# Performance work log

Measured on AMD Instinct MI355X. Metric: run time of the kernel, lower is better.

The kernel has to match this reference:

```python
import jax, jax.numpy as jnp
import numpy as np

EMBED = 1024
HEADS = 16
HEAD_DIM = EMBED // HEADS


def setup_inputs() -> dict:
    key = jax.random.key(0)
    ks = jax.random.split(key, 11)
    B, L, E = 2, 2048, EMBED
    s = 1.0 / np.sqrt(E)
    return {
        "query": jax.random.normal(ks[0], (B, L, E), jnp.float32),
        "key": jax.random.normal(ks[1], (B, L, E), jnp.float32),
        "value": jax.random.normal(ks[2], (B, L, E), jnp.float32),
        "Wq": jax.random.normal(ks[3], (E, E), jnp.float32) * s,
        "bq": jax.random.normal(ks[4], (E,), jnp.float32) * s,
        "Wk": jax.random.normal(ks[5], (E, E), jnp.float32) * s,
        "bk": jax.random.normal(ks[6], (E,), jnp.float32) * s,
        "Wv": jax.random.normal(ks[7], (E, E), jnp.float32) * s,
        "bv": jax.random.normal(ks[8], (E,), jnp.float32) * s,
        "Wo": jax.random.normal(ks[9], (E, E), jnp.float32) * s,
        "bo": jax.random.normal(ks[10], (E,), jnp.float32) * s,
    }


def reference(query, key, value, Wq, bq, Wk, bk, Wv, bv, Wo, bo):
    B, Lq, E = query.shape
    Lk = key.shape[1]
    # Linear projections (torch Linear: x @ W.T + b)
    q = (query @ Wq.T + bq).reshape(B, Lq, HEADS, HEAD_DIM).transpose(0, 2, 1, 3)
    k = (key @ Wk.T + bk).reshape(B, Lk, HEADS, HEAD_DIM).transpose(0, 2, 1, 3)
    v = (value @ Wv.T + bv).reshape(B, Lk, HEADS, HEAD_DIM).transpose(0, 2, 1, 3)
    # NOTE: original scales by sqrt(embed_size), not sqrt(head_dim)
    energy = jnp.einsum("bhqd,bhkd->bhqk", q, k) / jnp.sqrt(jnp.float32(E))
    attn = jax.nn.softmax(energy, axis=-1)
    out = jnp.einsum("bhqk,bhkd->bhqd", attn, v)  # [B,H,Lq,D]
    out = out.transpose(0, 2, 1, 3).reshape(B, Lq, E)
    return out @ Wo.T + bo
```

## Files before the change

### kernel.cpp

```cpp
#include <hip/hip_runtime.h>
#include <hip/hip_bf16.h>


typedef __attribute__((ext_vector_type(4))) float f32x4;
typedef __attribute__((ext_vector_type(16))) float f32x16;
typedef __attribute__((ext_vector_type(8))) short bf16x8;
typedef __attribute__((ext_vector_type(4))) short bf16x4;
typedef __attribute__((ext_vector_type(2))) unsigned int u32x2;

static __device__ __forceinline__ unsigned short f2bf(float f) {
  union { float f; unsigned int u; } a; a.f = f;
  unsigned int u = a.u;
  u += 0x7FFFu + ((u >> 16) & 1u);
  return (unsigned short)(u >> 16);
}

static __device__ __forceinline__ unsigned packrn(float lo, float hi) {
  __hip_bfloat162 h = __float22bfloat162_rn(float2{lo, hi});
  union { __hip_bfloat162 h; unsigned u; } c; c.h = h;
  return c.u;
}

static __device__ __forceinline__ unsigned pack2(float lo, float hi) {
  unsigned a = __float_as_uint(lo) + 0x8000u;
  unsigned b = __float_as_uint(hi) + 0x8000u;
  return __builtin_amdgcn_perm(b, a, 0x07060302);
}

static __device__ __forceinline__ unsigned xchg32(unsigned x) {
  u32x2 r = __builtin_amdgcn_permlane32_swap(x, x, false, false);
  return x ^ r[0] ^ r[1];
}

#define AS1(p) ((const __attribute__((address_space(1))) void*)(p))
#define AS3(p) ((__attribute__((address_space(3))) void*)(p))

__global__ __launch_bounds__(256) void cvt_kernel(
    const float* __restrict__ q, const float* __restrict__ k, const float* __restrict__ v,
    const float* __restrict__ wq, const float* __restrict__ wk, const float* __restrict__ wv,
    const float* __restrict__ wo, short* __restrict__ ws) {
  long i = (long)blockIdx.x * 256 + threadIdx.x;
  long e = i * 8;
  const float* src; long off;
  if (e < 12582912) {
    int s = (int)(e >> 22);
    src = s == 0 ? q : (s == 1 ? k : v);
    off = e & 4194303;
  } else {
    long e2 = e - 12582912;
    int s = (int)(e2 >> 20);
    src = s == 0 ? wq : (s == 1 ? wk : (s == 2 ? wv : wo));
    off = e2 & 1048575;
  }
  f32x4 a = *(const f32x4*)(src + off);
  f32x4 b = *(const f32x4*)(src + off + 4);
  bf16x8 o;
  o[0] = (short)f2bf(a[0]); o[1] = (short)f2bf(a[1]);
  o[2] = (short)f2bf(a[2]); o[3] = (short)f2bf(a[3]);
  o[4] = (short)f2bf(b[0]); o[5] = (short)f2bf(b[1]);
  o[6] = (short)f2bf(b[2]); o[7] = (short)f2bf(b[3]);
  *(bf16x8*)(ws + e) = o;
}

__device__ __forceinline__ void gemm_tile(const short* __restrict__ A, const short* __restrict__ B,
                                          int m0, int n0, f32x4 acc[4][4],
                                          short* As, short* Bs) {
  const int t = threadIdx.x;
  const int lane = t & 63, w = t >> 6;
  const int wr = w >> 1, wc = w & 1;
  const int x = lane & 15, g = lane >> 4;
  const int lr = lane >> 3;
  const int lc = ((lane & 7) ^ lr) * 8;
  const int rswz = (x & 7) * 8;

#pragma unroll
  for (int fm = 0; fm < 4; fm++)
#pragma unroll
    for (int fn = 0; fn < 4; fn++)
#pragma unroll
      for (int r = 0; r < 4; r++) acc[fm][fn][r] = 0.0f;

  for (int k0 = 0; k0 < 1024; k0 += 64) {
    __syncthreads();
#pragma unroll
    for (int i = 0; i < 4; i++) {
      int ch = w * 4 + i;
      const short* ga = A + (long)(m0 + ch * 8 + lr) * 1024 + k0 + lc;
      __builtin_amdgcn_global_load_lds(AS1(ga), AS3(As + ch * 512), 16, 0, 0);
      const short* gb = B + (long)(n0 + ch * 8 + lr) * 1024 + k0 + lc;
      __builtin_amdgcn_global_load_lds(AS1(gb), AS3(Bs + ch * 512), 16, 0, 0);
    }
    __syncthreads();
#pragma unroll
    for (int ks = 0; ks < 2; ks++) {
      bf16x8 af[4], bfv[4];
#pragma unroll
      for (int f = 0; f < 4; f++) {
        int c = (ks * 32 + g * 8) ^ rswz;
        af[f]  = *(const bf16x8*)(As + (wr * 64 + f * 16 + x) * 64 + c);
        bfv[f] = *(const bf16x8*)(Bs + (wc * 64 + f * 16 + x) * 64 + c);
      }
#pragma unroll
      for (int fm = 0; fm < 4; fm++)
#pragma unroll
        for (int fn = 0; fn < 4; fn++)
          acc[fm][fn] = __builtin_amdgcn_mfma_f32_16x16x32_bf16(af[fm], bfv[fn], acc[fm][fn], 0, 0, 0);
    }
  }
}

__global__ __launch_bounds__(256) void proj_kernel(
    const short* __restrict__ Xq, const short* __restrict__ Xk, const short* __restrict__ Xv,
    const short* __restrict__ Wq, const short* __restrict__ Wk, const short* __restrict__ Wv,
    const float* __restrict__ bq, const float* __restrict__ bk, const float* __restrict__ bv,
    short* __restrict__ Qo, short* __restrict__ Ko, short* __restrict__ Vto) {
  __shared__ short As[8192], Bs[8192];
  const int lin = blockIdx.z * 256 + blockIdx.y * 8 + blockIdx.x;
  const int wgid = (lin & 7) * 96 + (lin >> 3);
  const int z = wgid >> 8;
  const int m0 = ((wgid >> 3) & 31) * 128, n0 = (wgid & 7) * 128;
  const short* A = z == 0 ? Xq : (z == 1 ? Xk : Xv);
  const short* B = z == 0 ? Wq : (z == 1 ? Wk : Wv);
  const float* bias = z == 0 ? bq : (z == 1 ? bk : bv);
  f32x4 acc[4][4];
  gemm_tile(A, B, m0, n0, acc, As, Bs);

  const int lane = threadIdx.x & 63, w = threadIdx.x >> 6;
  const int wr = w >> 1, wc = w & 1, x = lane & 15, g = lane >> 4;

  if (z == 0) {
    const float scale = 0.04508422002778f;
#pragma unroll
    for (int fn = 0; fn < 4; fn++) {
      int n = n0 + wc * 64 + fn * 16 + x;
      float bb = bias[n];
      int h = n >> 6, d = n & 63;
#pragma unroll
      for (int fm = 0; fm < 4; fm++) {
        int mb = m0 + wr * 64 + fm * 16 + g * 4;
#pragma unroll
        for (int r = 0; r < 4; r++) {
          int m = mb + r;
          int b = m >> 11, l = m & 2047;
          float val = (acc[fm][fn][r] + bb) * scale;
          Qo[((long)((b * 16 + h) * 2048 + l)) * 64 + d] = (short)f2bf(val);
        }
      }
    }
  } else if (z == 1) {
#pragma unroll
    for (int fn = 0; fn < 4; fn++) {
      int n = n0 + wc * 64 + fn * 16 + x;
      float bb = bias[n];
      int h = n >> 6, d = n & 63;
#pragma unroll
      for (int fm = 0; fm < 4; fm++) {
        int mb = m0 + wr * 64 + fm * 16 + g * 4;
#pragma unroll
        for (int r = 0; r < 4; r++) {
          int m = mb + r;
          int b = m >> 11, kv = m & 2047;
          int ds = d ^ ((kv & 7) << 3);
          Ko[((long)((b * 16 + h) * 2048 + kv)) * 64 + ds] = (short)f2bf(acc[fm][fn][r] + bb);
        }
      }
    }
  } else {
#pragma unroll
    for (int fn = 0; fn < 4; fn++) {
      int n = n0 + wc * 64 + fn * 16 + x;
      float bb = bias[n];
      int h = n >> 6, d = n & 63;
#pragma unroll
      for (int fm = 0; fm < 4; fm++) {
        int mb = m0 + wr * 64 + fm * 16 + g * 4;
        int b = mb >> 11, kvb = mb & 2047;
        bf16x4 pk;
#pragma unroll
        for (int r = 0; r < 4; r++) pk[r] = (short)f2bf(acc[fm][fn][r] + bb);
        int kvs = (kvb & ~63) | ((kvb & 63) ^ ((d & 7) << 3));
        *(bf16x4*)(Vto + ((long)((b * 16 + h) * 64 + d)) * 2048 + kvs) = pk;
      }
    }
  }
}

__global__ __launch_bounds__(128, 2) void attn_kernel(
    const short* __restrict__ Qg, const short* __restrict__ Kg,
    const short* __restrict__ Vtg, short* __restrict__ Og) {
  __shared__ __align__(16) short Kl[2][4096];
  __shared__ __align__(16) short Vl[2][4096];
  const int t = threadIdx.x, w = t >> 6, lane = t & 63;
  const int col = lane & 31, hi = lane >> 5;
  const int lin = blockIdx.y * 32 + blockIdx.x;
  const int wgid = (lin & 7) * 128 + (lin >> 3);
  const int bh = wgid >> 5;
  const int q0 = (wgid & 31) * 64 + w * 32;
  const long hb = (long)bh * 2048 * 64;
  const int swz = (col & 7) * 8;

  bf16x8 qf[4];
#pragma unroll
  for (int ksl = 0; ksl < 4; ksl++)
    qf[ksl] = *(const bf16x8*)(Qg + hb + (long)(q0 + col) * 64 + ksl * 16 + hi * 8);

  union { unsigned u[4]; bf16x8 v; } onesf;
#pragma unroll
  for (int i = 0; i < 4; i++) onesf.u[i] = 0x3F803F80u;

  f32x16 o0, o1, o2;
#pragma unroll
  for (int i = 0; i < 16; i++) { o0[i] = 0.0f; o1[i] = 0.0f; o2[i] = 0.0f; }

  auto stage = [&](int buf, int kv0) {
#pragma unroll
    for (int it = 0; it < 4; it++) {
      int c = it * 128 + w * 64 + lane;
      const short* gk = Kg + hb + (long)kv0 * 64 + (long)c * 8;
      __builtin_amdgcn_global_load_lds(AS1(gk), AS3(&Kl[buf][(it * 128 + w * 64) * 8]), 16, 0, 0);
      const short* gv = Vtg + hb + (long)(c >> 3) * 2048 + kv0 + (c & 7) * 8;
      __builtin_amdgcn_global_load_lds(AS1(gv), AS3(&Vl[buf][(it * 128 + w * 64) * 8]), 16, 0, 0);
    }
  };

  stage(0, 0);
  __syncthreads();

  for (int ti = 0; ti < 32; ti++) {
    const int buf = ti & 1;
    if (ti < 31) stage(buf ^ 1, (ti + 1) * 64);

    f32x16 s0, s1;
#pragma unroll
    for (int i = 0; i < 16; i++) { s0[i] = 0.0f; s1[i] = 0.0f; }
    __builtin_amdgcn_s_setprio(1);
#pragma unroll
    for (int ksl = 0; ksl < 4; ksl++) {
      int dcol = (ksl * 16 + hi * 8) ^ swz;
      bf16x8 a0 = *(const bf16x8*)(&Kl[buf][col * 64 + dcol]);
      bf16x8 a1 = *(const bf16x8*)(&Kl[buf][(col + 32) * 64 + dcol]);
      s0 = __builtin_amdgcn_mfma_f32_32x32x16_bf16(a0, qf[ksl], s0, 0, 0, 0);
      s1 = __builtin_amdgcn_mfma_f32_32x32x16_bf16(a1, qf[ksl], s1, 0, 0, 0);
    }
    __builtin_amdgcn_s_setprio(0);

#pragma unroll
    for (int i = 0; i < 16; i++) { s0[i] = __builtin_amdgcn_exp2f(s0[i]); }
#pragma unroll
    for (int i = 0; i < 16; i++) { s1[i] = __builtin_amdgcn_exp2f(s1[i]); }

#define PVSTEP(SEL, KS)                                                       \
    {                                                                         \
      unsigned pkA0 = packrn(SEL[8 * ((KS) & 1) + 0], SEL[8 * ((KS) & 1) + 1]); \
      unsigned pkA1 = packrn(SEL[8 * ((KS) & 1) + 2], SEL[8 * ((KS) & 1) + 3]); \
      unsigned pkB0 = packrn(SEL[8 * ((KS) & 1) + 4], SEL[8 * ((KS) & 1) + 5]); \
      unsigned pkB1 = packrn(SEL[8 * ((KS) & 1) + 6], SEL[8 * ((KS) & 1) + 7]); \
      unsigned own0 = hi ? pkB0 : pkA0, own1 = hi ? pkB1 : pkA1;              \
      unsigned oth0 = hi ? pkA0 : pkB0, oth1 = hi ? pkA1 : pkB1;              \
      unsigned r0 = xchg32(oth0);                                             \
      unsigned r1 = xchg32(oth1);                                             \
      union { unsigned u[4]; bf16x8 v; } pb;                                  \
      pb.u[0] = hi ? r0 : own0; pb.u[1] = hi ? r1 : own1;                     \
      pb.u[2] = hi ? own0 : r0; pb.u[3] = hi ? own1 : r1;                     \
      const int vcol = ((KS) * 16 + hi * 8) ^ swz;                            \
      bf16x8 vb0 = *(const bf16x8*)(&Vl[buf][col * 64 + vcol]);               \
      bf16x8 vb1 = *(const bf16x8*)(&Vl[buf][(col + 32) * 64 + vcol]);        \
      __builtin_amdgcn_s_setprio(1);                                          \
      o0 = __builtin_amdgcn_mfma_f32_32x32x16_bf16(vb0, pb.v, o0, 0, 0, 0);   \
      o1 = __builtin_amdgcn_mfma_f32_32x32x16_bf16(vb1, pb.v, o1, 0, 0, 0);   \
      o2 = __builtin_amdgcn_mfma_f32_32x32x16_bf16(onesf.v, pb.v, o2, 0, 0, 0); \
      __builtin_amdgcn_s_setprio(0);                                          \
    }
    PVSTEP(s0, 0)
    PVSTEP(s0, 1)
    PVSTEP(s1, 2)
    PVSTEP(s1, 3)
#undef PVSTEP

    __syncthreads();
  }

  const float inv = 1.0f / o2[0];
  const int b = bh >> 4, h = bh & 15;
  const long base = ((long)(b * 2048 + q0 + col) * 16 + h) * 64;
#pragma unroll
  for (int dh = 0; dh < 2; dh++) {
#pragma unroll
    for (int g2 = 0; g2 < 4; g2++) {
      float x0 = (dh ? o1[g2 * 4 + 0] : o0[g2 * 4 + 0]) * inv;
      float x1 = (dh ? o1[g2 * 4 + 1] : o0[g2 * 4 + 1]) * inv;
      float x2 = (dh ? o1[g2 * 4 + 2] : o0[g2 * 4 + 2]) * inv;
      float x3 = (dh ? o1[g2 * 4 + 3] : o0[g2 * 4 + 3]) * inv;
      u32x2 rr;
      rr[0] = (unsigned)f2bf(x0) | ((unsigned)f2bf(x1) << 16);
      rr[1] = (unsigned)f2bf(x2) | ((unsigned)f2bf(x3) << 16);
      int d = dh * 32 + g2 * 8 + hi * 4;
      *(u32x2*)(Og + base + d) = rr;
    }
  }
}

__global__ __launch_bounds__(256) void out_kernel(
    const short* __restrict__ O, const short* __restrict__ Wo,
    const float* __restrict__ bo, float* __restrict__ out) {
  __shared__ short As[8192], Bs[8192];
  const int lin = blockIdx.y * 8 + blockIdx.x;
  const int wgid = (lin & 7) * 32 + (lin >> 3);
  const int m0 = (wgid >> 3) * 128, n0 = (wgid & 7) * 128;
  f32x4 acc[4][4];
  gemm_tile(O, Wo, m0, n0, acc, As, Bs);
  const int lane = threadIdx.x & 63, w = threadIdx.x >> 6;
  const int wr = w >> 1, wc = w & 1, x = lane & 15, g = lane >> 4;
#pragma unroll
  for (int fn = 0; fn < 4; fn++) {
    int n = n0 + wc * 64 + fn * 16 + x;
    float bb = bo[n];
#pragma unroll
    for (int fm = 0; fm < 4; fm++) {
      int mb = m0 + wr * 64 + fm * 16 + g * 4;
#pragma unroll
      for (int r = 0; r < 4; r++)
        out[(long)(mb + r) * 1024 + n] = acc[fm][fn][r] + bb;
    }
  }
}

extern "C" void kernel_launch(void* const* d_in, const int* in_sizes, int n_in,
                              void* d_out, int out_size, void* d_ws, size_t ws_size,
                              hipStream_t stream) {
  const float* q  = (const float*)d_in[0];
  const float* k  = (const float*)d_in[1];
  const float* v  = (const float*)d_in[2];
  const float* wq = (const float*)d_in[3];
  const float* bq = (const float*)d_in[4];
  const float* wk = (const float*)d_in[5];
  const float* bk = (const float*)d_in[6];
  const float* wv = (const float*)d_in[7];
  const float* bv = (const float*)d_in[8];
  const float* wo = (const float*)d_in[9];
  const float* bo = (const float*)d_in[10];

  short* ws  = (short*)d_ws;
  short* Xq  = ws;
  short* Xk  = Xq + 4194304;
  short* Xv  = Xk + 4194304;
  short* Wqb = Xv + 4194304;
  short* Wkb = Wqb + 1048576;
  short* Wvb = Wkb + 1048576;
  short* Wob = Wvb + 1048576;
  short* Qb  = Wob + 1048576;
  short* Kb  = Qb + 4194304;
  short* Vtb = Kb + 4194304;
  short* Ob  = Vtb + 4194304;

  cvt_kernel<<<8192, 256, 0, stream>>>(q, k, v, wq, wk, wv, wo, ws);
  dim3 gp(8, 32, 3);
  proj_kernel<<<gp, 256, 0, stream>>>(Xq, Xk, Xv, Wqb, Wkb, Wvb, bq, bk, bv, Qb, Kb, Vtb);
  dim3 ga(32, 32);
  attn_kernel<<<ga, 128, 0, stream>>>(Qb, Kb, Vtb, Ob);
  dim3 gf(8, 32);
  out_kernel<<<gf, 256, 0, stream>>>(Ob, Wob, bo, (float*)d_out);
}
```

Baseline: 147.6 us.

## Split attention KV range across two workgroups and combine partials in new kernel

Attention workgroups now use 256 threads covering 128 query rows, each handling half of the key/value sequence (split-K over KV). Unnormalized partial outputs go to fp16 buffers and row sums to a float buffer, and a new combine kernel adds the halves, normalizes, and writes bf16 output in the layout the output projection expects. The aim is shorter per-workgroup loops, higher occupancy and better latency hiding. The cost is an extra kernel launch, extra global traffic for partials, and fp16 range risk on unnormalized sums. Partials reuse the dead Xq/Xk workspace region.

Result: no change. 148.2 us (+0.4%).

```diff
diff --git a/kernel.cpp b/kernel.cpp
--- a/kernel.cpp
+++ b/kernel.cpp
@@ -7,6 +7,7 @@
 typedef __attribute__((ext_vector_type(8))) short bf16x8;
 typedef __attribute__((ext_vector_type(4))) short bf16x4;
 typedef __attribute__((ext_vector_type(2))) unsigned int u32x2;
+typedef __attribute__((ext_vector_type(4))) unsigned int u32x4;
 
 static __device__ __forceinline__ unsigned short f2bf(float f) {
   union { float f; unsigned int u; } a; a.f = f;
@@ -19,12 +20,6 @@
   __hip_bfloat162 h = __float22bfloat162_rn(float2{lo, hi});
   union { __hip_bfloat162 h; unsigned u; } c; c.h = h;
   return c.u;
-}
-
-static __device__ __forceinline__ unsigned pack2(float lo, float hi) {
-  unsigned a = __float_as_uint(lo) + 0x8000u;
-  unsigned b = __float_as_uint(hi) + 0x8000u;
-  return __builtin_amdgcn_perm(b, a, 0x07060302);
 }
 
 static __device__ __forceinline__ unsigned xchg32(unsigned x) {
@@ -185,9 +180,10 @@
   }
 }
 
-__global__ __launch_bounds__(128, 2) void attn_kernel(
+__global__ __launch_bounds__(256, 4) void attn_kernel(
     const short* __restrict__ Qg, const short* __restrict__ Kg,
-    const short* __restrict__ Vtg, short* __restrict__ Og) {
+    const short* __restrict__ Vtg, _Float16* __restrict__ Op0,
+    _Float16* __restrict__ Op1, float* __restrict__ Lp) {
   __shared__ __align__(16) short Kl[2][4096];
   __shared__ __align__(16) short Vl[2][4096];
   const int t = threadIdx.x, w = t >> 6, lane = t & 63;
@@ -195,7 +191,10 @@
   const int lin = blockIdx.y * 32 + blockIdx.x;
   const int wgid = (lin & 7) * 128 + (lin >> 3);
   const int bh = wgid >> 5;
-  const int q0 = (wgid & 31) * 64 + w * 32;
+  const int rem = wgid & 31;
+  const int q0 = (rem >> 1) * 128 + w * 32;
+  const int s = rem & 1;
+  const int kvb = s * 1024;
   const long hb = (long)bh * 2048 * 64;
   const int swz = (col & 7) * 8;
 
@@ -214,21 +213,22 @@
 
   auto stage = [&](int buf, int kv0) {
 #pragma unroll
-    for (int it = 0; it < 4; it++) {
-      int c = it * 128 + w * 64 + lane;
+    for (int it = 0; it < 2; it++) {
+      int cb = it * 256 + w * 64;
+      int c = cb + lane;
       const short* gk = Kg + hb + (long)kv0 * 64 + (long)c * 8;
-      __builtin_amdgcn_global_load_lds(AS1(gk), AS3(&Kl[buf][(it * 128 + w * 64) * 8]), 16, 0, 0);
+      __builtin_amdgcn_global_load_lds(AS1(gk), AS3(&Kl[buf][cb * 8]), 16, 0, 0);
       const short* gv = Vtg + hb + (long)(c >> 3) * 2048 + kv0 + (c & 7) * 8;
-      __builtin_amdgcn_global_load_lds(AS1(gv), AS3(&Vl[buf][(it * 128 + w * 64) * 8]), 16, 0, 0);
+      __builtin_amdgcn_global_load_lds(AS1(gv), AS3(&Vl[buf][cb * 8]), 16, 0, 0);
     }
   };
 
-  stage(0, 0);
+  stage(0, kvb);
   __syncthreads();
 
-  for (int ti = 0; ti < 32; ti++) {
+  for (int ti = 0; ti < 16; ti++) {
     const int buf = ti & 1;
-    if (ti < 31) stage(buf ^ 1, (ti + 1) * 64);
+    if (ti < 15) stage(buf ^ 1, kvb + (ti + 1) * 64);
 
     f32x16 s0, s1;
 #pragma unroll
@@ -280,24 +280,43 @@
     __syncthreads();
   }
 
-  const float inv = 1.0f / o2[0];
-  const int b = bh >> 4, h = bh & 15;
-  const long base = ((long)(b * 2048 + q0 + col) * 16 + h) * 64;
+  const int qrow = q0 + col;
+  _Float16* Ops = s ? Op1 : Op0;
+  const long pbase = ((long)bh * 2048 + qrow) * 64;
 #pragma unroll
   for (int dh = 0; dh < 2; dh++) {
 #pragma unroll
     for (int g2 = 0; g2 < 4; g2++) {
-      float x0 = (dh ? o1[g2 * 4 + 0] : o0[g2 * 4 + 0]) * inv;
-      float x1 = (dh ? o1[g2 * 4 + 1] : o0[g2 * 4 + 1]) * inv;
-      float x2 = (dh ? o1[g2 * 4 + 2] : o0[g2 * 4 + 2]) * inv;
-      float x3 = (dh ? o1[g2 * 4 + 3] : o0[g2 * 4 + 3]) * inv;
-      u32x2 rr;
-      rr[0] = (unsigned)f2bf(x0) | ((unsigned)f2bf(x1) << 16);
-      rr[1] = (unsigned)f2bf(x2) | ((unsigned)f2bf(x3) << 16);
+      float x0 = dh ? o1[g2 * 4 + 0] : o0[g2 * 4 + 0];
+      float x1 = dh ? o1[g2 * 4 + 1] : o0[g2 * 4 + 1];
+      float x2 = dh ? o1[g2 * 4 + 2] : o0[g2 * 4 + 2];
+      float x3 = dh ? o1[g2 * 4 + 3] : o0[g2 * 4 + 3];
+      union { _Float16 h[4]; u32x2 u; } ph;
+      ph.h[0] = (_Float16)x0; ph.h[1] = (_Float16)x1;
+      ph.h[2] = (_Float16)x2; ph.h[3] = (_Float16)x3;
       int d = dh * 32 + g2 * 8 + hi * 4;
-      *(u32x2*)(Og + base + d) = rr;
-    }
-  }
+      *(u32x2*)(Ops + pbase + d) = ph.u;
+    }
+  }
+  if (hi == 0) Lp[s * 65536 + bh * 2048 + qrow] = o2[0];
+}
+
+__global__ __launch_bounds__(256) void comb_kernel(
+    const _Float16* __restrict__ Op0, const _Float16* __restrict__ Op1,
+    const float* __restrict__ Lp, short* __restrict__ Ob) {
+  long e = ((long)blockIdx.x * 256 + threadIdx.x) * 8;
+  int row = (int)(e >> 6);
+  float inv = 1.0f / (Lp[row] + Lp[65536 + row]);
+  union { u32x4 u; _Float16 h[8]; } a, b2;
+  a.u  = *(const u32x4*)(Op0 + e);
+  b2.u = *(const u32x4*)(Op1 + e);
+  bf16x8 o;
+#pragma unroll
+  for (int i = 0; i < 8; i++)
+    o[i] = (short)f2bf(((float)a.h[i] + (float)b2.h[i]) * inv);
+  int bh = row >> 11, q = row & 2047, d = (int)(e & 63);
+  int b = bh >> 4, h = bh & 15;
+  *(bf16x8*)(Ob + ((long)((b * 2048 + q) * 16 + h)) * 64 + d) = o;
 }
 
 __global__ __launch_bounds__(256) void out_kernel(
@@ -353,11 +372,16 @@
   short* Vtb = Kb + 4194304;
   short* Ob  = Vtb + 4194304;
 
+  _Float16* Op0 = (_Float16*)ws;
+  _Float16* Op1 = Op0 + 4194304;
+  float*    Lp  = (float*)(ws + 8388608);
+
   cvt_kernel<<<8192, 256, 0, stream>>>(q, k, v, wq, wk, wv, wo, ws);
   dim3 gp(8, 32, 3);
   proj_kernel<<<gp, 256, 0, stream>>>(Xq, Xk, Xv, Wqb, Wkb, Wvb, bq, bk, bv, Qb, Kb, Vtb);
   dim3 ga(32, 32);
-  attn_kernel<<<ga, 128, 0, stream>>>(Qb, Kb, Vtb, Ob);
+  attn_kernel<<<ga, 256, 0, stream>>>(Qb, Kb, Vtb, Op0, Op1, Lp);
+  comb_kernel<<<2048, 256, 0, stream>>>(Op0, Op1, Lp, Ob);
   dim3 gf(8, 32);
   out_kernel<<<gf, 256, 0, stream>>>(Ob, Wob, bo, (float*)d_out);
 }
```
